# Optimization experiments

Measured on AMD Instinct MI355X. Metric: run time of the kernel, lower is better.

## Reference

```python
import jax, jax.numpy as jnp
import numpy as np

B, C, H, W = 8, 256, 64, 64   # batch, num_hiddens, spatial
N, D = 1024, 256              # n_embed, embedding_dim
TEMP = 1.0                    # temp_init


def setup_inputs() -> dict:
    key = jax.random.key(0)
    k1, k2, k3 = jax.random.split(key, 3)
    z = jax.random.normal(k1, (B, C, H, W), dtype=jnp.float32)
    # 1x1 conv == per-pixel linear: weight [n_embed, num_hiddens], bias [n_embed]
    proj_w = jax.random.normal(k2, (N, C), dtype=jnp.float32) * 0.02
    proj_b = jnp.zeros((N,), dtype=jnp.float32)
    embed = jax.random.normal(k3, (N, D), dtype=jnp.float32) * 0.02
    return {"z": z, "proj_w": proj_w, "proj_b": proj_b, "embed": embed}


def reference(z, proj_w, proj_b, embed):
    # logits = Conv2d(num_hiddens, n_embed, 1)(z)  -> [b, n, h, w]
    logits = jnp.einsum('bchw,nc->bnhw', z, proj_w) + proj_b[None, :, None, None]
    # argmax_softmax (straight-through) over the codebook axis (dim=1), tau=TEMP
    y_soft = jax.nn.softmax(logits / TEMP, axis=1)
    ind = jnp.argmax(y_soft, axis=1)  # [b, h, w]
    y_hard = jax.nn.one_hot(ind, N, axis=1, dtype=logits.dtype)  # [b, n, h, w]
    soft_one_hot = y_hard - jax.lax.stop_gradient(y_soft) + y_soft
    # z_q = einsum('b n h w, n d -> b d h w', soft_one_hot, embed)
    z_q = jnp.einsum('bnhw,nd->bdhw', soft_one_hot, embed)
    diff = jnp.zeros((1,), dtype=logits.dtype)
    return (z_q, diff, ind)
```

## Files before the change

### kernel.cpp

```cpp
#include <hip/hip_runtime.h>
#include <math.h>

#define HWP 4096
#define CCH 256
#define NN  1024
#define DD  256
#define ZQ_SIZE (8 * DD * HWP)
#define MARGIN 2e-3f
#define WLCAP 4096
#define NCH 8
#define PXB 8

typedef _Float16 h8 __attribute__((ext_vector_type(8)));
typedef float    f4 __attribute__((ext_vector_type(4)));

__global__ __launch_bounds__(256) void split_w_k(
    const float* __restrict__ w, _Float16* __restrict__ whS,
    int* __restrict__ wcount, unsigned long long* __restrict__ fin,
    int* __restrict__ pgdone)
{
    const int t = blockIdx.x * 256 + threadIdx.x;
    if (t == 0) *wcount = 0;
    if (t < WLCAP) fin[t] = 0ULL;
    if (t < 512)  pgdone[t] = 0;
    const int l = t & 63;
    const int frag = t >> 6;
    const int kc = frag & 7, r16 = frag >> 3;
    const int row = r16 * 16 + (l & 15);
    const int c   = kc * 32 + (l >> 4) * 8;
    const float* src = w + (size_t)row * CCH + c;
    _Float16 hv[8];
#pragma unroll
    for (int j = 0; j < 8; ++j) hv[j] = (_Float16)src[j];
    *(h8*)(whS + (size_t)t * 8) = *(const h8*)hv;
}

__global__ __launch_bounds__(512, 4) void mfma_gemm_k(
    const float* __restrict__ z,
    const _Float16* __restrict__ whS,
    const float* __restrict__ bias, const float* __restrict__ embed,
    int* __restrict__ wcount, int* __restrict__ wlist,
    float* __restrict__ out)
{
    __shared__ __align__(16) char smem[71680];
    __shared__ int indsh2[64];
    float* s_best = (float*)(smem + 65536);
    float* s_sec  = (float*)(smem + 67584);
    int*   s_idx  = (int*)  (smem + 69632);

    const int tid = threadIdx.x;
    const int l   = tid & 63;
    const int wv  = tid >> 6;
    const int mh  = wv >> 2;
    const int ng  = wv & 3;
    const int c15 = l & 15, g = l >> 4;
    const int pix0 = blockIdx.x * 64;
    const int b = pix0 >> 12, p0 = pix0 & 4095;

    {
        const int px = tid & 63;
        const int wv2 = tid >> 6;
        const int p16 = px >> 4;
        const float* zb = z + (size_t)b * CCH * HWP + p0 + px;
#pragma unroll
        for (int it = 0; it < 4; ++it) {
            const int cg = wv2 * 4 + it;
            const int c = cg * 8;
            float xv[8];
#pragma unroll
            for (int i = 0; i < 8; ++i) xv[i] = zb[(size_t)(c + i) * HWP];
            _Float16 hv[8], lv[8];
#pragma unroll
            for (int i = 0; i < 8; ++i) {
                const _Float16 h = (_Float16)xv[i];
                hv[i] = h;
                lv[i] = (_Float16)(xv[i] - (float)h);
            }
            const int kc = cg >> 2;
            const int lane = (px & 15) + 16 * (cg & 3);
            const int off = ((p16 * 8 + kc) * 64 + lane) * 16;
            *(h8*)(smem + off)         = *(const h8*)hv;
            *(h8*)(smem + 32768 + off) = *(const h8*)lv;
        }
    }
    __syncthreads();

    float best[8], sec[8]; int bidx[8];
#pragma unroll
    for (int s = 0; s < 8; ++s) { best[s] = -INFINITY; sec[s] = -INFINITY; bidx[s] = 0; }

#pragma unroll 1
    for (int nt = 0; nt < 4; ++nt) {
        const int n0 = nt * 256 + ng * 64;
        const int r16_0 = n0 >> 4;
        f4 acc[2][4];
#pragma unroll
        for (int mf = 0; mf < 2; ++mf)
#pragma unroll
            for (int nf = 0; nf < 4; ++nf) acc[mf][nf] = (f4)0.f;

#pragma unroll 2
        for (int kc = 0; kc < 8; ++kc) {
            h8 ah[2], al[2], bh[4];
#pragma unroll
            for (int mf = 0; mf < 2; ++mf) {
                const int ao = (((mh * 2 + mf) * 8 + kc) * 64 + l) * 16;
                ah[mf] = *(const h8*)(smem + ao);
                al[mf] = *(const h8*)(smem + 32768 + ao);
            }
#pragma unroll
            for (int nf = 0; nf < 4; ++nf) {
                const size_t bo = (((size_t)(r16_0 + nf) * 8 + kc) * 64 + l) * 8;
                bh[nf] = *(const h8*)(whS + bo);
            }
#pragma unroll
            for (int mf = 0; mf < 2; ++mf)
#pragma unroll
                for (int nf = 0; nf < 4; ++nf) {
                    acc[mf][nf] = __builtin_amdgcn_mfma_f32_16x16x32_f16(ah[mf], bh[nf], acc[mf][nf], 0, 0, 0);
                    acc[mf][nf] = __builtin_amdgcn_mfma_f32_16x16x32_f16(al[mf], bh[nf], acc[mf][nf], 0, 0, 0);
                }
        }
#pragma unroll
        for (int nf = 0; nf < 4; ++nf) {
            const int n_abs = n0 + nf * 16 + c15;
            const float bv = bias[n_abs];
#pragma unroll
            for (int mf = 0; mf < 2; ++mf)
#pragma unroll
                for (int r = 0; r < 4; ++r) {
                    const float v = acc[mf][nf][r] + bv;
                    const int s = mf * 4 + r;
                    if (v > best[s]) { sec[s] = best[s]; best[s] = v; bidx[s] = n_abs; }
                    else if (v > sec[s]) sec[s] = v;
                }
        }
    }

#pragma unroll
    for (int d = 1; d < 16; d <<= 1) {
#pragma unroll
        for (int s = 0; s < 8; ++s) {
            const float ob = __shfl_xor(best[s], d, 64);
            const float os = __shfl_xor(sec[s], d, 64);
            const int   oi = __shfl_xor(bidx[s], d, 64);
            if (ob > best[s])       { sec[s] = fmaxf(best[s], os); best[s] = ob; bidx[s] = oi; }
            else if (ob == best[s]) { sec[s] = ob; bidx[s] = (oi < bidx[s]) ? oi : bidx[s]; }
            else                    { sec[s] = fmaxf(sec[s], ob); }
        }
    }
#pragma unroll
    for (int s = 0; s < 8; ++s) {
        if (c15 == s) {
            const int px = (mh * 2 + (s >> 2)) * 16 + g * 4 + (s & 3);
            s_best[wv * 64 + px] = best[s];
            s_sec [wv * 64 + px] = sec[s];
            s_idx [wv * 64 + px] = bidx[s];
        }
    }
    __syncthreads();
    if (tid < 64) {
        const int wb = (tid >> 5) * 4;
        float b0 = s_best[wb * 64 + tid], s0 = s_sec[wb * 64 + tid]; int i0 = s_idx[wb * 64 + tid];
#pragma unroll
        for (int c = 1; c < 4; ++c) {
            const float ob = s_best[(wb + c) * 64 + tid], os = s_sec[(wb + c) * 64 + tid];
            const int   oi = s_idx [(wb + c) * 64 + tid];
            if (ob > b0 || (ob == b0 && oi < i0)) { s0 = fmaxf(b0, os); b0 = ob; i0 = oi; }
            else                                  { s0 = fmaxf(s0, ob); }
        }
        const int pix = pix0 + tid;
        indsh2[tid] = i0;
        out[ZQ_SIZE + 1 + pix] = (float)i0;
        if (b0 - s0 < MARGIN) {
            const int pos = atomicAdd(wcount, 1);
            if (pos < WLCAP) wlist[pos] = pix;
        }
    }
    if (blockIdx.x == 0 && tid == 0) out[ZQ_SIZE] = 0.0f;
    __syncthreads();

    float (*tile)[257] = (float (*)[257])smem;
    const int lq = tid & 63, wq = tid >> 6;
    const int l32 = tid & 31, dq = tid >> 5;
#pragma unroll 1
    for (int pp = 0; pp < 2; ++pp) {
#pragma unroll
        for (int it = 0; it < 4; ++it) {
            const int pl = it * 8 + wq;
            const int row = indsh2[pp * 32 + pl];
            const float4 e = *(const float4*)(embed + (size_t)row * DD + lq * 4);
            tile[pl][lq * 4 + 0] = e.x;
            tile[pl][lq * 4 + 1] = e.y;
            tile[pl][lq * 4 + 2] = e.z;
            tile[pl][lq * 4 + 3] = e.w;
        }
        __syncthreads();
        float* outz = out + (size_t)b * DD * HWP + p0 + pp * 32;
#pragma unroll
        for (int dd = 0; dd < 16; ++dd) {
            const int d = dd * 16 + dq;
            outz[(size_t)d * HWP + l32] = tile[l32][d];
        }
        __syncthreads();
    }
}

__global__ __launch_bounds__(256) void fixup_k(
    const float* __restrict__ z, const float* __restrict__ w,
    const float* __restrict__ bias, const float* __restrict__ embed,
    const int* __restrict__ wcount, const int* __restrict__ wlist,
    unsigned long long* __restrict__ fin, int* __restrict__ pgdone,
    float* __restrict__ out)
{
    __shared__ float zsh[PXB][256];
    __shared__ float m_v[4][PXB];
    __shared__ int   m_i[4][PXB];
    __shared__ int   s_idx[PXB];
    __shared__ int   s_fin;

    const int tid = threadIdx.x;
    const int l = tid & 63, wv = tid >> 6;
    const int c15 = l & 15, q = l >> 4;
    int nw = *wcount;
    if (nw > WLCAP) nw = WLCAP;
    if (nw < 0) nw = 0;
    const int npg = (nw + PXB - 1) / PXB;
    const int ntask = npg * NCH;

    for (int t = blockIdx.x; t < ntask; t += 1024) {
        const int pg = t >> 3, ck = t & 7;
        const int e0 = pg * PXB;
        const int npx = (nw - e0 < PXB) ? (nw - e0) : PXB;
        int pixv[PXB];
#pragma unroll
        for (int px = 0; px < PXB; ++px)
            pixv[px] = wlist[e0 + ((px < npx) ? px : (npx - 1))];

        __syncthreads();
#pragma unroll
        for (int px = 0; px < PXB; ++px) {
            const int pix = pixv[px];
            const int b = pix >> 12, p = pix & 4095;
            zsh[px][tid] = z[((size_t)b * CCH + tid) * HWP + p];
        }
        __syncthreads();

        float best[PXB]; int bi[PXB];
#pragma unroll
        for (int px = 0; px < PXB; ++px) { best[px] = -INFINITY; bi[px] = 0; }

#pragma unroll
        for (int g16 = 0; g16 < 2; ++g16) {
            const int row = ck * 128 + wv * 32 + g16 * 16 + c15;
            const float* wr = w + (size_t)row * CCH + q * 64;
            float part[PXB];
#pragma unroll
            for (int px = 0; px < PXB; ++px) part[px] = 0.f;
#pragma unroll
            for (int j = 0; j < 16; ++j) {
                const float4 w4 = *(const float4*)(wr + j * 4);
#pragma unroll
                for (int px = 0; px < PXB; ++px) {
                    const float4 z4 = *(const float4*)&zsh[px][q * 64 + j * 4];
                    part[px] = fmaf(w4.x, z4.x, part[px]);
                    part[px] = fmaf(w4.y, z4.y, part[px]);
                    part[px] = fmaf(w4.z, z4.z, part[px]);
                    part[px] = fmaf(w4.w, z4.w, part[px]);
                }
            }
            const float bv = bias[row];
#pragma unroll
            for (int px = 0; px < PXB; ++px) {
                float pv = part[px];
                pv += __shfl_xor(pv, 16, 64);
                pv += __shfl_xor(pv, 32, 64);
                const float v = pv + bv;
                if (v > best[px]) { best[px] = v; bi[px] = row; }
            }
        }
#pragma unroll
        for (int d = 1; d < 16; d <<= 1) {
#pragma unroll
            for (int px = 0; px < PXB; ++px) {
                const float ob = __shfl_xor(best[px], d, 64);
                const int   oi = __shfl_xor(bi[px], d, 64);
                if (ob > best[px] || (ob == best[px] && oi < bi[px])) { best[px] = ob; bi[px] = oi; }
            }
        }
        if (l == 0) {
#pragma unroll
            for (int px = 0; px < PXB; ++px) { m_v[wv][px] = best[px]; m_i[wv][px] = bi[px]; }
        }
        __syncthreads();
        if (tid < npx) {
            float v = m_v[0][tid]; int i = m_i[0][tid];
#pragma unroll
            for (int t2 = 1; t2 < 4; ++t2)
                if (m_v[t2][tid] > v || (m_v[t2][tid] == v && m_i[t2][tid] < i)) { v = m_v[t2][tid]; i = m_i[t2][tid]; }
            const unsigned int s = __float_as_uint(v);
            const unsigned int key = (s & 0x80000000u) ? ~s : (s | 0x80000000u);
            const unsigned long long enc =
                ((unsigned long long)key << 32) | (unsigned long long)(~(unsigned int)i);
            atomicMax(&fin[e0 + tid], enc);
        }
        __syncthreads();
        if (tid == 0) {
            __threadfence();
            const int old = atomicAdd(&pgdone[pg], 1);
            s_fin = (old == NCH - 1) ? 1 : 0;
        }
        __syncthreads();
        if (s_fin) {
            if (tid < npx) {
                const unsigned long long cur = atomicMax(&fin[e0 + tid], 0ULL);
                const int idx = (int)(~(unsigned int)cur);
                s_idx[tid] = idx;
                out[ZQ_SIZE + 1 + pixv[tid]] = (float)idx;
            }
            __syncthreads();
            for (int px = 0; px < npx; ++px) {
                const int pix = pixv[px];
                const int b = pix >> 12, p = pix & 4095;
                out[((size_t)b * DD + tid) * HWP + p] = embed[(size_t)s_idx[px] * DD + tid];
            }
        }
    }
}

extern "C" void kernel_launch(void* const* d_in, const int* in_sizes, int n_in,
                              void* d_out, int out_size, void* d_ws, size_t ws_size,
                              hipStream_t stream) {
    const float* z     = (const float*)d_in[0];
    const float* w     = (const float*)d_in[1];
    const float* bias  = (const float*)d_in[2];
    const float* embed = (const float*)d_in[3];
    float* out = (float*)d_out;

    _Float16* whS = (_Float16*)d_ws;
    int* wcount = (int*)((char*)d_ws + 524288);
    int* wlist  = (int*)((char*)d_ws + 524544);
    unsigned long long* fin = (unsigned long long*)((char*)d_ws + 540928);
    int* pgdone = (int*)((char*)d_ws + 573696);

    hipLaunchKernelGGL(split_w_k,   dim3(128), dim3(256), 0, stream, w, whS, wcount, fin, pgdone);
    hipLaunchKernelGGL(mfma_gemm_k, dim3(512), dim3(512), 0, stream,
                       z, whS, bias, embed, wcount, wlist, out);
    hipLaunchKernelGGL(fixup_k,     dim3(1024), dim3(256), 0, stream,
                       z, w, bias, embed, wcount, wlist, fin, pgdone, out);
}
```

Before: 200.9 us.

## Process all codebook rows per pixel group in one block, drop atomic merge

The fixup kernel no longer splits the 1024 codebook rows across 8 blocks per pixel group. Each 512-thread block now scans all rows for its 8 pixels and reduces across 8 waves in shared memory. This removes the 64-bit atomicMax merge, the completion counters and the workspace clearing in split_w_k. In exchange there are fewer parallel tasks when the fallback list is short, and each block does a longer serial loop, with the weight row chunk preloaded into registers.

```diff
diff --git a/kernel.cpp b/kernel.cpp
--- a/kernel.cpp
+++ b/kernel.cpp
@@ -8,7 +8,6 @@
 #define ZQ_SIZE (8 * DD * HWP)
 #define MARGIN 2e-3f
 #define WLCAP 4096
-#define NCH 8
 #define PXB 8
 
 typedef _Float16 h8 __attribute__((ext_vector_type(8)));
@@ -16,13 +15,10 @@
 
 __global__ __launch_bounds__(256) void split_w_k(
     const float* __restrict__ w, _Float16* __restrict__ whS,
-    int* __restrict__ wcount, unsigned long long* __restrict__ fin,
-    int* __restrict__ pgdone)
+    int* __restrict__ wcount)
 {
+    if (blockIdx.x == 0 && threadIdx.x == 0) *wcount = 0;
     const int t = blockIdx.x * 256 + threadIdx.x;
-    if (t == 0) *wcount = 0;
-    if (t < WLCAP) fin[t] = 0ULL;
-    if (t < 512)  pgdone[t] = 0;
     const int l = t & 63;
     const int frag = t >> 6;
     const int kc = frag & 7, r16 = frag >> 3;
@@ -206,18 +202,16 @@
     }
 }
 
-__global__ __launch_bounds__(256) void fixup_k(
+__global__ __launch_bounds__(512) void fixup_k(
     const float* __restrict__ z, const float* __restrict__ w,
     const float* __restrict__ bias, const float* __restrict__ embed,
     const int* __restrict__ wcount, const int* __restrict__ wlist,
-    unsigned long long* __restrict__ fin, int* __restrict__ pgdone,
     float* __restrict__ out)
 {
     __shared__ float zsh[PXB][256];
-    __shared__ float m_v[4][PXB];
-    __shared__ int   m_i[4][PXB];
+    __shared__ float m_v[8][PXB];
+    __shared__ int   m_i[8][PXB];
     __shared__ int   s_idx[PXB];
-    __shared__ int   s_fin;
 
     const int tid = threadIdx.x;
     const int l = tid & 63, wv = tid >> 6;
@@ -226,10 +220,8 @@
     if (nw > WLCAP) nw = WLCAP;
     if (nw < 0) nw = 0;
     const int npg = (nw + PXB - 1) / PXB;
-    const int ntask = npg * NCH;
-
-    for (int t = blockIdx.x; t < ntask; t += 1024) {
-        const int pg = t >> 3, ck = t & 7;
+
+    for (int pg = blockIdx.x; pg < npg; pg += 512) {
         const int e0 = pg * PXB;
         const int npx = (nw - e0 < PXB) ? (nw - e0) : PXB;
         int pixv[PXB];
@@ -239,10 +231,12 @@
 
         __syncthreads();
 #pragma unroll
-        for (int px = 0; px < PXB; ++px) {
+        for (int it = 0; it < (PXB * 256) / 512; ++it) {
+            const int i = it * 512 + tid;
+            const int px = i >> 8, c = i & 255;
             const int pix = pixv[px];
             const int b = pix >> 12, p = pix & 4095;
-            zsh[px][tid] = z[((size_t)b * CCH + tid) * HWP + p];
+            zsh[px][c] = z[((size_t)b * CCH + c) * HWP + p];
         }
         __syncthreads();
 
@@ -250,23 +244,25 @@
 #pragma unroll
         for (int px = 0; px < PXB; ++px) { best[px] = -INFINITY; bi[px] = 0; }
 
-#pragma unroll
-        for (int g16 = 0; g16 < 2; ++g16) {
-            const int row = ck * 128 + wv * 32 + g16 * 16 + c15;
+#pragma unroll 1
+        for (int g16 = 0; g16 < 8; ++g16) {
+            const int row = wv * 128 + g16 * 16 + c15;
             const float* wr = w + (size_t)row * CCH + q * 64;
+            float4 w4[16];
+#pragma unroll
+            for (int j = 0; j < 16; ++j) w4[j] = *(const float4*)(wr + j * 4);
             float part[PXB];
 #pragma unroll
             for (int px = 0; px < PXB; ++px) part[px] = 0.f;
 #pragma unroll
             for (int j = 0; j < 16; ++j) {
-                const float4 w4 = *(const float4*)(wr + j * 4);
 #pragma unroll
                 for (int px = 0; px < PXB; ++px) {
                     const float4 z4 = *(const float4*)&zsh[px][q * 64 + j * 4];
-                    part[px] = fmaf(w4.x, z4.x, part[px]);
-                    part[px] = fmaf(w4.y, z4.y, part[px]);
-                    part[px] = fmaf(w4.z, z4.z, part[px]);
-                    part[px] = fmaf(w4.w, z4.w, part[px]);
+                    part[px] = fmaf(w4[j].x, z4.x, part[px]);
+                    part[px] = fmaf(w4[j].y, z4.y, part[px]);
+                    part[px] = fmaf(w4[j].z, z4.z, part[px]);
+                    part[px] = fmaf(w4[j].w, z4.w, part[px]);
                 }
             }
             const float bv = bias[row];
@@ -296,33 +292,20 @@
         if (tid < npx) {
             float v = m_v[0][tid]; int i = m_i[0][tid];
 #pragma unroll
-            for (int t2 = 1; t2 < 4; ++t2)
-                if (m_v[t2][tid] > v || (m_v[t2][tid] == v && m_i[t2][tid] < i)) { v = m_v[t2][tid]; i = m_i[t2][tid]; }
-            const unsigned int s = __float_as_uint(v);
-            const unsigned int key = (s & 0x80000000u) ? ~s : (s | 0x80000000u);
-            const unsigned long long enc =
-                ((unsigned long long)key << 32) | (unsigned long long)(~(unsigned int)i);
-            atomicMax(&fin[e0 + tid], enc);
-        }
-        __syncthreads();
-        if (tid == 0) {
-            __threadfence();
-            const int old = atomicAdd(&pgdone[pg], 1);
-            s_fin = (old == NCH - 1) ? 1 : 0;
-        }
-        __syncthreads();
-        if (s_fin) {
-            if (tid < npx) {
-                const unsigned long long cur = atomicMax(&fin[e0 + tid], 0ULL);
-                const int idx = (int)(~(unsigned int)cur);
-                s_idx[tid] = idx;
-                out[ZQ_SIZE + 1 + pixv[tid]] = (float)idx;
-            }
-            __syncthreads();
-            for (int px = 0; px < npx; ++px) {
+            for (int w2 = 1; w2 < 8; ++w2)
+                if (m_v[w2][tid] > v || (m_v[w2][tid] == v && m_i[w2][tid] < i)) { v = m_v[w2][tid]; i = m_i[w2][tid]; }
+            s_idx[tid] = i;
+            out[ZQ_SIZE + 1 + pixv[tid]] = (float)i;
+        }
+        __syncthreads();
+#pragma unroll
+        for (int pp = 0; pp < PXB; pp += 2) {
+            const int px = pp + (tid >> 8);
+            const int d = tid & 255;
+            if (px < npx) {
                 const int pix = pixv[px];
                 const int b = pix >> 12, p = pix & 4095;
-                out[((size_t)b * DD + tid) * HWP + p] = embed[(size_t)s_idx[px] * DD + tid];
+                out[((size_t)b * DD + d) * HWP + p] = embed[(size_t)s_idx[px] * DD + d];
             }
         }
     }
@@ -340,12 +323,10 @@
     _Float16* whS = (_Float16*)d_ws;
     int* wcount = (int*)((char*)d_ws + 524288);
     int* wlist  = (int*)((char*)d_ws + 524544);
-    unsigned long long* fin = (unsigned long long*)((char*)d_ws + 540928);
-    int* pgdone = (int*)((char*)d_ws + 573696);
-
-    hipLaunchKernelGGL(split_w_k,   dim3(128), dim3(256), 0, stream, w, whS, wcount, fin, pgdone);
+
+    hipLaunchKernelGGL(split_w_k,   dim3(128), dim3(256), 0, stream, w, whS, wcount);
     hipLaunchKernelGGL(mfma_gemm_k, dim3(512), dim3(512), 0, stream,
                        z, whS, bias, embed, wcount, wlist, out);
-    hipLaunchKernelGGL(fixup_k,     dim3(1024), dim3(256), 0, stream,
-                       z, w, bias, embed, wcount, wlist, fin, pgdone, out);
+    hipLaunchKernelGGL(fixup_k,     dim3(512), dim3(512), 0, stream,
+                       z, w, bias, embed, wcount, wlist, out);
 }
```

Result: slower. 554.1 us (+175.8%).
